# Kernel optimization log

Hardware: AMD Instinct MI355X
Metric: run time of the kernel (lower is better)

The kernel has to match this reference:

```python
import jax, jax.numpy as jnp
import numpy as np

NOT_EPSILON = 1.0
B, K, Q, T = 2, 512, 512, 128


def swishmax(x, axis):
    # x * exp(x - max) normalized by sum(|.|) + 1 along `axis`
    xexp = x * jnp.exp(x - jnp.max(x, axis=axis, keepdims=True))
    return xexp / (jnp.sum(jnp.abs(xexp), axis=axis, keepdims=True) + NOT_EPSILON)


def setup_inputs() -> dict:
    key = jax.random.key(0)
    ks = jax.random.split(key, 8)
    scale = 1.0 / np.sqrt(T)
    return {
        "query_tokens": jax.random.normal(ks[0], (B, Q, T), dtype=jnp.float32),
        "key_tokens": jax.random.normal(ks[1], (B, K, T), dtype=jnp.float32),
        "value_tokens": jax.random.normal(ks[2], (B, K, T), dtype=jnp.float32),
        "Wk": jax.random.normal(ks[3], (T, T), dtype=jnp.float32) * scale,
        "Wq": jax.random.normal(ks[4], (T, T), dtype=jnp.float32) * scale,
        "Wv": jax.random.normal(ks[5], (T, T), dtype=jnp.float32) * scale,
        "Wl": jax.random.normal(ks[6], (T, T), dtype=jnp.float32) * scale,
        "Wo": jax.random.normal(ks[7], (T, T), dtype=jnp.float32) * scale,
    }


def reference(query_tokens, key_tokens, value_tokens, Wk, Wq, Wv, Wl, Wo):
    lin = lambda x, W: jnp.einsum('...t,ut->...u', x, W)  # nn.Linear(bias=False): x @ W.T
    k = lin(key_tokens, Wk)       # [B, K, T]
    q = lin(query_tokens, Wq)     # [B, Q, T]
    # outer-product broadcast over tokens: [B, K, Q, T]
    attention_raw = k[..., :, None, :] * q[..., None, :, :]
    attention_logits = lin(attention_raw, Wl)            # [B, K, Q, T]
    attention_scale = swishmax(attention_logits, axis=-2)  # normalize over Q (dim=-2)
    v = lin(value_tokens, Wv)     # [B, K, T]
    values_scaled = v[..., :, None, :] * attention_scale  # [B, K, Q, T]
    value_sum = values_scaled.sum(axis=-3)                # sum over K -> [B, Q, T]
    return lin(value_sum, Wo)
```

## Files before the change

### kernel.cpp

```cpp
#include <hip/hip_runtime.h>


using f16    = _Float16;
using f16x8  = __attribute__((ext_vector_type(8)))  f16;
using f32x16 = __attribute__((ext_vector_type(16))) float;

#define LOG2E 1.4426950408889634f

__device__ __forceinline__ float exp2b(float x) {
  return __builtin_amdgcn_exp2f(x);
}

__device__ __forceinline__ f16x8 cvt8(float4 a, float4 b) {
  f16x8 r;
  r[0]=(f16)a.x; r[1]=(f16)a.y; r[2]=(f16)a.z; r[3]=(f16)a.w;
  r[4]=(f16)b.x; r[5]=(f16)b.y; r[6]=(f16)b.z; r[7]=(f16)b.w;
  return r;
}

__global__ __launch_bounds__(256, 2) void k1_proj(
    const float* __restrict__ q_tok, const float* __restrict__ k_tok,
    const float* __restrict__ v_tok, const float* __restrict__ Wq,
    const float* __restrict__ Wk,    const float* __restrict__ Wv,
    f16* __restrict__ qh, float* __restrict__ kls, float* __restrict__ vf,
    float* __restrict__ vsum)
{
  {
    const int idx = blockIdx.x*256 + threadIdx.x;
    const float4 z = make_float4(0.f,0.f,0.f,0.f);
    for (int j = idx; j < 32768; j += 48*256) ((float4*)vsum)[j] = z;
  }

  const int gid    = blockIdx.x;
  const int tensor = gid >> 4;
  const int sub    = gid & 15;
  const int b      = sub >> 3;
  const int rt     = sub & 7;
  const float* X = tensor==0 ? q_tok : (tensor==1 ? k_tok : v_tok);
  const float* W = tensor==0 ? Wq    : (tensor==1 ? Wk    : Wv);

  const int tid = threadIdx.x;
  const int w = tid >> 6, lane = tid & 63;
  const int l31 = lane & 31, lhi = lane >> 5;
  const int rbase = rt*64 + (w>>1)*32;
  const int cbase = (w&1)*64;

  f32x16 C0, C1;
  #pragma unroll
  for (int i=0;i<16;++i){ C0[i]=0.f; C1[i]=0.f; }

  #pragma unroll
  for (int kc=0; kc<8; ++kc) {
    const float* ap = X + (size_t)(b*512 + rbase + l31)*128 + kc*16 + 8*lhi;
    f16x8 a = cvt8(*(const float4*)ap, *(const float4*)(ap+4));
    const float* bp0 = W + (size_t)(cbase + l31)*128 + kc*16 + 8*lhi;
    f16x8 b0 = cvt8(*(const float4*)bp0, *(const float4*)(bp0+4));
    C0 = __builtin_amdgcn_mfma_f32_32x32x16_f16(a, b0, C0, 0, 0, 0);
    const float* bp1 = bp0 + 32*128;
    f16x8 b1 = cvt8(*(const float4*)bp1, *(const float4*)(bp1+4));
    C1 = __builtin_amdgcn_mfma_f32_32x32x16_f16(a, b1, C1, 0, 0, 0);
  }

  #pragma unroll
  for (int us=0; us<2; ++us) {
    #pragma unroll
    for (int r=0; r<16; ++r) {
      const int row = rbase + (r&3) + 8*(r>>2) + 4*lhi;
      const int col = cbase + us*32 + l31;
      const float val = us ? C1[r] : C0[r];
      const size_t idx = (size_t)(b*512 + row)*128 + col;
      if (tensor==0)      qh[idx]  = (f16)val;
      else if (tensor==1) kls[idx] = val * LOG2E;
      else                vf[idx]  = val;
    }
  }
}

__global__ __launch_bounds__(512, 2) void k2_main(
    const f16* __restrict__ qh, const float* __restrict__ kls,
    const float* __restrict__ vf, const float* __restrict__ Wl,
    float* __restrict__ vsum)
{
  const int gid  = blockIdx.x;
  const int b    = gid >> 7;
  const int half = (gid >> 6) & 1;
  const int grp  = gid & 63;
  const int kk0  = grp * 8;

  const int tid = threadIdx.x;
  const int w = tid >> 6, lane = tid & 63;
  const int l31 = lane & 31, lhi = lane >> 5;
  const int ubase = half * 64;
  const int qbase = w * 64;

  __shared__ f16    Bl[2][64][136];
  __shared__ float2 red[2][8][64];

  const int bu  = tid >> 3;
  const int btc = tid & 7;
  const float* wlr = Wl + (size_t)(ubase + bu)*128 + btc*16;
  const float4 wl0 = *(const float4*)(wlr);
  const float4 wl1 = *(const float4*)(wlr+4);
  const float4 wl2 = *(const float4*)(wlr+8);
  const float4 wl3 = *(const float4*)(wlr+12);

  const float* kbase = kls + (size_t)(b*512 + kk0)*128 + btc*16;
  const f16*   abase = qh  + (size_t)(b*512 + qbase + l31)*128 + 8*lhi;
  const float* vbase = vf  + (size_t)(b*512 + kk0)*128 + ubase;

  f32x16 acc[2][2];
  #pragma unroll
  for (int i=0;i<16;++i){ acc[0][0][i]=0.f; acc[0][1][i]=0.f;
                          acc[1][0][i]=0.f; acc[1][1][i]=0.f; }

  {
    const float4 k0 = *(const float4*)(kbase);
    const float4 k1 = *(const float4*)(kbase+4);
    const float4 k2 = *(const float4*)(kbase+8);
    const float4 k3 = *(const float4*)(kbase+12);
    float4 a0 = make_float4(wl0.x*k0.x, wl0.y*k0.y, wl0.z*k0.z, wl0.w*k0.w);
    float4 a1 = make_float4(wl1.x*k1.x, wl1.y*k1.y, wl1.z*k1.z, wl1.w*k1.w);
    float4 a2 = make_float4(wl2.x*k2.x, wl2.y*k2.y, wl2.z*k2.z, wl2.w*k2.w);
    float4 a3 = make_float4(wl3.x*k3.x, wl3.y*k3.y, wl3.z*k3.z, wl3.w*k3.w);
    *(f16x8*)(&Bl[0][bu][btc*16])     = cvt8(a0, a1);
    *(f16x8*)(&Bl[0][bu][btc*16 + 8]) = cvt8(a2, a3);
  }
  float4 n0 = *(const float4*)(kbase+128);
  float4 n1 = *(const float4*)(kbase+132);
  float4 n2 = *(const float4*)(kbase+136);
  float4 n3 = *(const float4*)(kbase+140);
  __syncthreads();

  for (int i=0; i<8; ++i) {
    const int cur = i & 1;

    const float v0 = vbase[i*128 + l31];
    const float v1 = vbase[i*128 + 32 + l31];

    if (i < 7) {
      float4 a0 = make_float4(wl0.x*n0.x, wl0.y*n0.y, wl0.z*n0.z, wl0.w*n0.w);
      float4 a1 = make_float4(wl1.x*n1.x, wl1.y*n1.y, wl1.z*n1.z, wl1.w*n1.w);
      float4 a2 = make_float4(wl2.x*n2.x, wl2.y*n2.y, wl2.z*n2.z, wl2.w*n2.w);
      float4 a3 = make_float4(wl3.x*n3.x, wl3.y*n3.y, wl3.z*n3.z, wl3.w*n3.w);
      *(f16x8*)(&Bl[cur^1][bu][btc*16])     = cvt8(a0, a1);
      *(f16x8*)(&Bl[cur^1][bu][btc*16 + 8]) = cvt8(a2, a3);
      if (i < 6) {
        const float* kp = kbase + (i+2)*128;
        n0 = *(const float4*)(kp);   n1 = *(const float4*)(kp+4);
        n2 = *(const float4*)(kp+8); n3 = *(const float4*)(kp+12);
      }
    }

    f32x16 C[2][2];
    #pragma unroll
    for (int j=0;j<16;++j){ C[0][0][j]=0.f; C[0][1][j]=0.f;
                            C[1][0][j]=0.f; C[1][1][j]=0.f; }
    #pragma unroll
    for (int kc=0; kc<8; ++kc) {
      f16x8 a0 = *(const f16x8*)(abase + kc*16);
      f16x8 a1 = *(const f16x8*)(abase + 32*128 + kc*16);
      #pragma unroll
      for (int us=0; us<2; ++us) {
        f16x8 bfr = *(const f16x8*)(&Bl[cur][us*32 + l31][kc*16 + 8*lhi]);
        C[0][us] = __builtin_amdgcn_mfma_f32_32x32x16_f16(a0, bfr, C[0][us], 0,0,0);
        C[1][us] = __builtin_amdgcn_mfma_f32_32x32x16_f16(a1, bfr, C[1][us], 0,0,0);
      }
    }

    float mx0a=-3.4e38f, mx0b=-3.4e38f, mx1a=-3.4e38f, mx1b=-3.4e38f;
    float s0a=0.f, s0b=0.f, s1a=0.f, s1b=0.f;
    #pragma unroll
    for (int qs=0; qs<2; ++qs)
      #pragma unroll
      for (int r=0; r<16; ++r) {
        const float y0 = C[qs][0][r], y1 = C[qs][1][r];
        const float p0 = y0 * exp2b(y0);
        const float p1 = y1 * exp2b(y1);
        C[qs][0][r] = p0; C[qs][1][r] = p1;
        if (r & 1) { mx0b=fmaxf(mx0b,y0); s0b+=fabsf(p0);
                     mx1b=fmaxf(mx1b,y1); s1b+=fabsf(p1); }
        else       { mx0a=fmaxf(mx0a,y0); s0a+=fabsf(p0);
                     mx1a=fmaxf(mx1a,y1); s1a+=fabsf(p1); }
      }
    float mx0 = fmaxf(mx0a,mx0b), mx1 = fmaxf(mx1a,mx1b);
    float sm0 = s0a+s0b,          sm1 = s1a+s1b;
    mx0 = fmaxf(mx0, __shfl_xor(mx0, 32));
    mx1 = fmaxf(mx1, __shfl_xor(mx1, 32));
    sm0 += __shfl_xor(sm0, 32);
    sm1 += __shfl_xor(sm1, 32);
    red[cur][w][lane] = lhi ? make_float2(mx1, sm1) : make_float2(mx0, sm0);

    __syncthreads();

    float M0=-3.4e38f, S0=0.f, M1=-3.4e38f, S1=0.f;
    #pragma unroll
    for (int ww=0; ww<8; ++ww) {
      const float2 t0 = red[cur][ww][l31];
      const float2 t1 = red[cur][ww][32+l31];
      M0 = fmaxf(M0, t0.x); S0 += t0.y;
      M1 = fmaxf(M1, t1.x); S1 += t1.y;
    }
    const float su0 = v0 / (S0 + LOG2E * exp2b(M0));
    const float su1 = v1 / (S1 + LOG2E * exp2b(M1));

    #pragma unroll
    for (int qs=0; qs<2; ++qs)
      #pragma unroll
      for (int r=0; r<16; ++r) {
        acc[qs][0][r] = fmaf(su0, C[qs][0][r], acc[qs][0][r]);
        acc[qs][1][r] = fmaf(su1, C[qs][1][r], acc[qs][1][r]);
      }

    __syncthreads();
  }

  #pragma unroll
  for (int qs=0; qs<2; ++qs)
    #pragma unroll
    for (int us=0; us<2; ++us)
      #pragma unroll
      for (int r=0; r<16; ++r) {
        const int q  = qbase + qs*32 + (r&3) + 8*(r>>2) + 4*lhi;
        const int uu = ubase + us*32 + l31;
        atomicAdd(vsum + (size_t)(b*512 + q)*128 + uu, acc[qs][us][r]);
      }
}

__global__ __launch_bounds__(256, 2) void k3_out(
    const float* __restrict__ vsum, const float* __restrict__ Wo,
    float* __restrict__ out)
{
  const int sub = blockIdx.x;
  const int b = sub >> 3, rt = sub & 7;
  const int tid = threadIdx.x;
  const int w = tid >> 6, lane = tid & 63;
  const int l31 = lane & 31, lhi = lane >> 5;
  const int rbase = rt*64 + (w>>1)*32;
  const int cbase = (w&1)*64;

  f32x16 C0, C1;
  #pragma unroll
  for (int i=0;i<16;++i){ C0[i]=0.f; C1[i]=0.f; }

  #pragma unroll
  for (int kc=0; kc<8; ++kc) {
    const float* ap = vsum + (size_t)(b*512 + rbase + l31)*128 + kc*16 + 8*lhi;
    f16x8 a = cvt8(*(const float4*)ap, *(const float4*)(ap+4));
    const float* bp0 = Wo + (size_t)(cbase + l31)*128 + kc*16 + 8*lhi;
    f16x8 b0 = cvt8(*(const float4*)bp0, *(const float4*)(bp0+4));
    C0 = __builtin_amdgcn_mfma_f32_32x32x16_f16(a, b0, C0, 0, 0, 0);
    const float* bp1 = bp0 + 32*128;
    f16x8 b1 = cvt8(*(const float4*)bp1, *(const float4*)(bp1+4));
    C1 = __builtin_amdgcn_mfma_f32_32x32x16_f16(a, b1, C1, 0, 0, 0);
  }

  #pragma unroll
  for (int us=0; us<2; ++us)
    #pragma unroll
    for (int r=0; r<16; ++r) {
      const int row = rbase + (r&3) + 8*(r>>2) + 4*lhi;
      const int col = cbase + us*32 + l31;
      out[(size_t)(b*512 + row)*128 + col] = us ? C1[r] : C0[r];
    }
}

extern "C" void kernel_launch(void* const* d_in, const int* in_sizes, int n_in,
                              void* d_out, int out_size, void* d_ws, size_t ws_size,
                              hipStream_t stream) {
  const float* q_tok = (const float*)d_in[0];
  const float* k_tok = (const float*)d_in[1];
  const float* v_tok = (const float*)d_in[2];
  const float* Wk    = (const float*)d_in[3];
  const float* Wq    = (const float*)d_in[4];
  const float* Wv    = (const float*)d_in[5];
  const float* Wl    = (const float*)d_in[6];
  const float* Wo    = (const float*)d_in[7];

  char* ws = (char*)d_ws;
  f16*   qh   = (f16*)  (ws);
  float* kls  = (float*)(ws + 262144);
  float* vf   = (float*)(ws + 786432);
  float* vsum = (float*)(ws + 1310720);

  k1_proj<<<48, 256, 0, stream>>>(q_tok, k_tok, v_tok, Wq, Wk, Wv, qh, kls, vf, vsum);
  k2_main<<<256, 512, 0, stream>>>(qh, kls, vf, Wl, vsum);
  k3_out<<<16, 256, 0, stream>>>(vsum, Wo, (float*)d_out);
}
```

Measured before the change: 141.9 us.

## Replace atomic vsum accumulation with fp16 partials and split u into quarters

The main kernel now splits the output feature dimension into four 32-wide slices instead of two, doubling the grid to 512 blocks and raising launch-bound occupancy. Per-block fp32 atomicAdd into vsum is replaced by plain fp16 stores into a 64-way partial buffer. The output kernel first reduces those partials in shared memory before the Wo GEMM, and the vsum zeroing in the projection kernel is removed. The aim is to drop atomic contention and the zero-init pass and to get more parallelism. In exchange it costs a larger workspace, extra partial-buffer traffic, a serial 64-step reduction in a 32-block kernel, and fp16 precision loss on the partial sums.

New measurement: 158.8 us. +11.9%, slower.

```diff
diff --git a/kernel.cpp b/kernel.cpp
--- a/kernel.cpp
+++ b/kernel.cpp
@@ -22,15 +22,8 @@
     const float* __restrict__ q_tok, const float* __restrict__ k_tok,
     const float* __restrict__ v_tok, const float* __restrict__ Wq,
     const float* __restrict__ Wk,    const float* __restrict__ Wv,
-    f16* __restrict__ qh, float* __restrict__ kls, float* __restrict__ vf,
-    float* __restrict__ vsum)
+    f16* __restrict__ qh, float* __restrict__ kls, float* __restrict__ vf)
 {
-  {
-    const int idx = blockIdx.x*256 + threadIdx.x;
-    const float4 z = make_float4(0.f,0.f,0.f,0.f);
-    for (int j = idx; j < 32768; j += 48*256) ((float4*)vsum)[j] = z;
-  }
-
   const int gid    = blockIdx.x;
   const int tensor = gid >> 4;
   const int sub    = gid & 15;
@@ -76,192 +69,178 @@
   }
 }
 
-__global__ __launch_bounds__(512, 2) void k2_main(
+__global__ __launch_bounds__(512, 4) void k2_main(
     const f16* __restrict__ qh, const float* __restrict__ kls,
     const float* __restrict__ vf, const float* __restrict__ Wl,
-    float* __restrict__ vsum)
+    f16* __restrict__ part)
 {
   const int gid  = blockIdx.x;
-  const int b    = gid >> 7;
-  const int half = (gid >> 6) & 1;
+  const int b    = gid >> 8;
+  const int uq   = (gid >> 6) & 3;
   const int grp  = gid & 63;
   const int kk0  = grp * 8;
 
   const int tid = threadIdx.x;
   const int w = tid >> 6, lane = tid & 63;
   const int l31 = lane & 31, lhi = lane >> 5;
-  const int ubase = half * 64;
+  const int ubase = uq * 32;
   const int qbase = w * 64;
 
-  __shared__ f16    Bl[2][64][136];
-  __shared__ float2 red[2][8][64];
-
-  const int bu  = tid >> 3;
-  const int btc = tid & 7;
-  const float* wlr = Wl + (size_t)(ubase + bu)*128 + btc*16;
+  __shared__ f16    Bl[2][32][136];
+  __shared__ float2 red[2][8][32];
+
+  const int bu  = tid >> 4;
+  const int btc = tid & 15;
+  const float* wlr = Wl + (size_t)(ubase + bu)*128 + btc*8;
   const float4 wl0 = *(const float4*)(wlr);
   const float4 wl1 = *(const float4*)(wlr+4);
-  const float4 wl2 = *(const float4*)(wlr+8);
-  const float4 wl3 = *(const float4*)(wlr+12);
-
-  const float* kbase = kls + (size_t)(b*512 + kk0)*128 + btc*16;
+
+  const float* kbase = kls + (size_t)(b*512 + kk0)*128 + btc*8;
   const f16*   abase = qh  + (size_t)(b*512 + qbase + l31)*128 + 8*lhi;
   const float* vbase = vf  + (size_t)(b*512 + kk0)*128 + ubase;
 
-  f32x16 acc[2][2];
-  #pragma unroll
-  for (int i=0;i<16;++i){ acc[0][0][i]=0.f; acc[0][1][i]=0.f;
-                          acc[1][0][i]=0.f; acc[1][1][i]=0.f; }
+  f32x16 acc[2];
+  #pragma unroll
+  for (int i=0;i<16;++i){ acc[0][i]=0.f; acc[1][i]=0.f; }
 
   {
     const float4 k0 = *(const float4*)(kbase);
     const float4 k1 = *(const float4*)(kbase+4);
-    const float4 k2 = *(const float4*)(kbase+8);
-    const float4 k3 = *(const float4*)(kbase+12);
     float4 a0 = make_float4(wl0.x*k0.x, wl0.y*k0.y, wl0.z*k0.z, wl0.w*k0.w);
     float4 a1 = make_float4(wl1.x*k1.x, wl1.y*k1.y, wl1.z*k1.z, wl1.w*k1.w);
-    float4 a2 = make_float4(wl2.x*k2.x, wl2.y*k2.y, wl2.z*k2.z, wl2.w*k2.w);
-    float4 a3 = make_float4(wl3.x*k3.x, wl3.y*k3.y, wl3.z*k3.z, wl3.w*k3.w);
-    *(f16x8*)(&Bl[0][bu][btc*16])     = cvt8(a0, a1);
-    *(f16x8*)(&Bl[0][bu][btc*16 + 8]) = cvt8(a2, a3);
+    *(f16x8*)(&Bl[0][bu][btc*8]) = cvt8(a0, a1);
   }
   float4 n0 = *(const float4*)(kbase+128);
   float4 n1 = *(const float4*)(kbase+132);
-  float4 n2 = *(const float4*)(kbase+136);
-  float4 n3 = *(const float4*)(kbase+140);
   __syncthreads();
 
   for (int i=0; i<8; ++i) {
     const int cur = i & 1;
 
     const float v0 = vbase[i*128 + l31];
-    const float v1 = vbase[i*128 + 32 + l31];
 
     if (i < 7) {
       float4 a0 = make_float4(wl0.x*n0.x, wl0.y*n0.y, wl0.z*n0.z, wl0.w*n0.w);
       float4 a1 = make_float4(wl1.x*n1.x, wl1.y*n1.y, wl1.z*n1.z, wl1.w*n1.w);
-      float4 a2 = make_float4(wl2.x*n2.x, wl2.y*n2.y, wl2.z*n2.z, wl2.w*n2.w);
-      float4 a3 = make_float4(wl3.x*n3.x, wl3.y*n3.y, wl3.z*n3.z, wl3.w*n3.w);
-      *(f16x8*)(&Bl[cur^1][bu][btc*16])     = cvt8(a0, a1);
-      *(f16x8*)(&Bl[cur^1][bu][btc*16 + 8]) = cvt8(a2, a3);
+      *(f16x8*)(&Bl[cur^1][bu][btc*8]) = cvt8(a0, a1);
       if (i < 6) {
         const float* kp = kbase + (i+2)*128;
         n0 = *(const float4*)(kp);   n1 = *(const float4*)(kp+4);
-        n2 = *(const float4*)(kp+8); n3 = *(const float4*)(kp+12);
       }
     }
 
-    f32x16 C[2][2];
-    #pragma unroll
-    for (int j=0;j<16;++j){ C[0][0][j]=0.f; C[0][1][j]=0.f;
-                            C[1][0][j]=0.f; C[1][1][j]=0.f; }
+    f32x16 C[2];
+    #pragma unroll
+    for (int j=0;j<16;++j){ C[0][j]=0.f; C[1][j]=0.f; }
     #pragma unroll
     for (int kc=0; kc<8; ++kc) {
       f16x8 a0 = *(const f16x8*)(abase + kc*16);
       f16x8 a1 = *(const f16x8*)(abase + 32*128 + kc*16);
-      #pragma unroll
-      for (int us=0; us<2; ++us) {
-        f16x8 bfr = *(const f16x8*)(&Bl[cur][us*32 + l31][kc*16 + 8*lhi]);
-        C[0][us] = __builtin_amdgcn_mfma_f32_32x32x16_f16(a0, bfr, C[0][us], 0,0,0);
-        C[1][us] = __builtin_amdgcn_mfma_f32_32x32x16_f16(a1, bfr, C[1][us], 0,0,0);
-      }
-    }
-
-    float mx0a=-3.4e38f, mx0b=-3.4e38f, mx1a=-3.4e38f, mx1b=-3.4e38f;
-    float s0a=0.f, s0b=0.f, s1a=0.f, s1b=0.f;
+      f16x8 bfr = *(const f16x8*)(&Bl[cur][l31][kc*16 + 8*lhi]);
+      C[0] = __builtin_amdgcn_mfma_f32_32x32x16_f16(a0, bfr, C[0], 0,0,0);
+      C[1] = __builtin_amdgcn_mfma_f32_32x32x16_f16(a1, bfr, C[1], 0,0,0);
+    }
+
+    float mxa=-3.4e38f, mxb=-3.4e38f, sa=0.f, sb=0.f;
     #pragma unroll
     for (int qs=0; qs<2; ++qs)
       #pragma unroll
       for (int r=0; r<16; ++r) {
-        const float y0 = C[qs][0][r], y1 = C[qs][1][r];
-        const float p0 = y0 * exp2b(y0);
-        const float p1 = y1 * exp2b(y1);
-        C[qs][0][r] = p0; C[qs][1][r] = p1;
-        if (r & 1) { mx0b=fmaxf(mx0b,y0); s0b+=fabsf(p0);
-                     mx1b=fmaxf(mx1b,y1); s1b+=fabsf(p1); }
-        else       { mx0a=fmaxf(mx0a,y0); s0a+=fabsf(p0);
-                     mx1a=fmaxf(mx1a,y1); s1a+=fabsf(p1); }
+        const float y = C[qs][r];
+        const float p = y * exp2b(y);
+        C[qs][r] = p;
+        if (r & 1) { mxb = fmaxf(mxb, y); sb += fabsf(p); }
+        else       { mxa = fmaxf(mxa, y); sa += fabsf(p); }
       }
-    float mx0 = fmaxf(mx0a,mx0b), mx1 = fmaxf(mx1a,mx1b);
-    float sm0 = s0a+s0b,          sm1 = s1a+s1b;
-    mx0 = fmaxf(mx0, __shfl_xor(mx0, 32));
-    mx1 = fmaxf(mx1, __shfl_xor(mx1, 32));
-    sm0 += __shfl_xor(sm0, 32);
-    sm1 += __shfl_xor(sm1, 32);
-    red[cur][w][lane] = lhi ? make_float2(mx1, sm1) : make_float2(mx0, sm0);
+    float mx = fmaxf(mxa, mxb);
+    float sm = sa + sb;
+    mx = fmaxf(mx, __shfl_xor(mx, 32));
+    sm += __shfl_xor(sm, 32);
+    if (lane < 32) red[cur][w][lane] = make_float2(mx, sm);
 
     __syncthreads();
 
-    float M0=-3.4e38f, S0=0.f, M1=-3.4e38f, S1=0.f;
+    float M = -3.4e38f, S = 0.f;
     #pragma unroll
     for (int ww=0; ww<8; ++ww) {
-      const float2 t0 = red[cur][ww][l31];
-      const float2 t1 = red[cur][ww][32+l31];
-      M0 = fmaxf(M0, t0.x); S0 += t0.y;
-      M1 = fmaxf(M1, t1.x); S1 += t1.y;
-    }
-    const float su0 = v0 / (S0 + LOG2E * exp2b(M0));
-    const float su1 = v1 / (S1 + LOG2E * exp2b(M1));
+      const float2 t = red[cur][ww][l31];
+      M = fmaxf(M, t.x); S += t.y;
+    }
+    const float su = v0 / (S + LOG2E * exp2b(M));
 
     #pragma unroll
     for (int qs=0; qs<2; ++qs)
       #pragma unroll
-      for (int r=0; r<16; ++r) {
-        acc[qs][0][r] = fmaf(su0, C[qs][0][r], acc[qs][0][r]);
-        acc[qs][1][r] = fmaf(su1, C[qs][1][r], acc[qs][1][r]);
-      }
+      for (int r=0; r<16; ++r)
+        acc[qs][r] = fmaf(su, C[qs][r], acc[qs][r]);
 
     __syncthreads();
   }
 
+  f16* pbase = part + ((size_t)(grp*2 + b)*512)*128 + ubase + l31;
   #pragma unroll
   for (int qs=0; qs<2; ++qs)
     #pragma unroll
-    for (int us=0; us<2; ++us)
-      #pragma unroll
-      for (int r=0; r<16; ++r) {
-        const int q  = qbase + qs*32 + (r&3) + 8*(r>>2) + 4*lhi;
-        const int uu = ubase + us*32 + l31;
-        atomicAdd(vsum + (size_t)(b*512 + q)*128 + uu, acc[qs][us][r]);
-      }
+    for (int r=0; r<16; ++r) {
+      const int q = qbase + qs*32 + (r&3) + 8*(r>>2) + 4*lhi;
+      pbase[(size_t)q*128] = (f16)acc[qs][r];
+    }
 }
 
 __global__ __launch_bounds__(256, 2) void k3_out(
-    const float* __restrict__ vsum, const float* __restrict__ Wo,
+    const f16* __restrict__ part, const float* __restrict__ Wo,
     float* __restrict__ out)
 {
-  const int sub = blockIdx.x;
-  const int b = sub >> 3, rt = sub & 7;
+  const int gid = blockIdx.x;
+  const int qt = gid >> 1, b = gid & 1;
+  const int rbase = qt * 32;
   const int tid = threadIdx.x;
+
+  __shared__ f16 vt[32][136];
+
+  {
+    const int q  = tid >> 3;
+    const int uc = tid & 7;
+    float s[16];
+    #pragma unroll
+    for (int j=0;j<16;++j) s[j] = 0.f;
+    const f16* pb = part + ((size_t)b*512 + rbase + q)*128 + uc*16;
+    for (int g=0; g<64; ++g) {
+      const f16x8 p0 = *(const f16x8*)(pb + (size_t)g*131072);
+      const f16x8 p1 = *(const f16x8*)(pb + (size_t)g*131072 + 8);
+      #pragma unroll
+      for (int j=0;j<8;++j) { s[j] += (float)p0[j]; s[8+j] += (float)p1[j]; }
+    }
+    f16x8 o0, o1;
+    #pragma unroll
+    for (int j=0;j<8;++j) { o0[j] = (f16)s[j]; o1[j] = (f16)s[8+j]; }
+    *(f16x8*)(&vt[q][uc*16])     = o0;
+    *(f16x8*)(&vt[q][uc*16 + 8]) = o1;
+  }
+  __syncthreads();
+
   const int w = tid >> 6, lane = tid & 63;
   const int l31 = lane & 31, lhi = lane >> 5;
-  const int rbase = rt*64 + (w>>1)*32;
-  const int cbase = (w&1)*64;
-
-  f32x16 C0, C1;
-  #pragma unroll
-  for (int i=0;i<16;++i){ C0[i]=0.f; C1[i]=0.f; }
+  const int cbase = w * 32;
+
+  f32x16 C;
+  #pragma unroll
+  for (int i=0;i<16;++i) C[i] = 0.f;
 
   #pragma unroll
   for (int kc=0; kc<8; ++kc) {
-    const float* ap = vsum + (size_t)(b*512 + rbase + l31)*128 + kc*16 + 8*lhi;
-    f16x8 a = cvt8(*(const float4*)ap, *(const float4*)(ap+4));
-    const float* bp0 = Wo + (size_t)(cbase + l31)*128 + kc*16 + 8*lhi;
-    f16x8 b0 = cvt8(*(const float4*)bp0, *(const float4*)(bp0+4));
-    C0 = __builtin_amdgcn_mfma_f32_32x32x16_f16(a, b0, C0, 0, 0, 0);
-    const float* bp1 = bp0 + 32*128;
-    f16x8 b1 = cvt8(*(const float4*)bp1, *(const float4*)(bp1+4));
-    C1 = __builtin_amdgcn_mfma_f32_32x32x16_f16(a, b1, C1, 0, 0, 0);
-  }
-
-  #pragma unroll
-  for (int us=0; us<2; ++us)
-    #pragma unroll
-    for (int r=0; r<16; ++r) {
-      const int row = rbase + (r&3) + 8*(r>>2) + 4*lhi;
-      const int col = cbase + us*32 + l31;
-      out[(size_t)(b*512 + row)*128 + col] = us ? C1[r] : C0[r];
-    }
+    f16x8 a = *(const f16x8*)(&vt[l31][kc*16 + 8*lhi]);
+    const float* bp = Wo + (size_t)(cbase + l31)*128 + kc*16 + 8*lhi;
+    f16x8 bfr = cvt8(*(const float4*)bp, *(const float4*)(bp+4));
+    C = __builtin_amdgcn_mfma_f32_32x32x16_f16(a, bfr, C, 0, 0, 0);
+  }
+
+  #pragma unroll
+  for (int r=0; r<16; ++r) {
+    const int row = rbase + (r&3) + 8*(r>>2) + 4*lhi;
+    const int col = cbase + l31;
+    out[(size_t)(b*512 + row)*128 + col] = C[r];
+  }
 }
 
 extern "C" void kernel_launch(void* const* d_in, const int* in_sizes, int n_in,
@@ -280,9 +259,9 @@
   f16*   qh   = (f16*)  (ws);
   float* kls  = (float*)(ws + 262144);
   float* vf   = (float*)(ws + 786432);
-  float* vsum = (float*)(ws + 1310720);
-
-  k1_proj<<<48, 256, 0, stream>>>(q_tok, k_tok, v_tok, Wq, Wk, Wv, qh, kls, vf, vsum);
-  k2_main<<<256, 512, 0, stream>>>(qh, kls, vf, Wl, vsum);
-  k3_out<<<16, 256, 0, stream>>>(vsum, Wo, (float*)d_out);
-}
+  f16*   part = (f16*)  (ws + 1310720);
+
+  k1_proj<<<48, 256, 0, stream>>>(q_tok, k_tok, v_tok, Wq, Wk, Wv, qh, kls, vf);
+  k2_main<<<512, 512, 0, stream>>>(qh, kls, vf, Wl, part);
+  k3_out<<<32, 256, 0, stream>>>(part, Wo, (float*)d_out);
+}
```
